# Optimization experiments

Hardware: AMD Instinct MI355X
Metric: run time of the kernel (lower is better)

Reference implementation:

```python
import jax, jax.numpy as jnp
import numpy as np

N_NODES = 50000

def setup_inputs() -> dict:
    key = jax.random.key(0)
    ks = jax.random.split(key, 8)
    input_dim, hidden_dim, output_dim = 128, 256, 64
    x = jax.random.normal(ks[0], (N_NODES, input_dim), dtype=jnp.float32)
    edge_index = jax.random.randint(ks[1], (2, 800000), 0, N_NODES, dtype=jnp.int64)
    s1 = 1.0 / np.sqrt(input_dim)
    s2 = 1.0 / np.sqrt(hidden_dim)
    W1 = jax.random.uniform(ks[2], (input_dim, hidden_dim), jnp.float32, -s1, s1)
    b1 = jax.random.uniform(ks[3], (hidden_dim,), jnp.float32, -s1, s1)
    W2 = jax.random.uniform(ks[4], (hidden_dim, hidden_dim), jnp.float32, -s2, s2)
    b2 = jax.random.uniform(ks[5], (hidden_dim,), jnp.float32, -s2, s2)
    Wc = jax.random.uniform(ks[6], (hidden_dim, output_dim), jnp.float32, -s2, s2)
    bc = jax.random.uniform(ks[7], (output_dim,), jnp.float32, -s2, s2)
    return {"x": x, "edge_index": edge_index, "W1": W1, "b1": b1,
            "W2": W2, "b2": b2, "Wc": Wc, "bc": bc}

def reference(x, edge_index, W1, b1, W2, b2, Wc, bc):
    src, dst = edge_index[0], edge_index[1]
    # GINConv (eps=0): h_i = (1+eps)*x_i + sum_{j->i} x_j
    aggr = jax.ops.segment_sum(x[src], dst, num_segments=N_NODES)  # [N, d_in]
    h = x + aggr
    # 2-layer MLP: Linear -> ReLU -> Linear
    h = jax.nn.relu(h @ W1 + b1) @ W2 + b2  # [N, hidden]
    # classifier on ReLU(conv output)
    return jax.nn.relu(h) @ Wc + bc  # [N, out]
```

## Files before the change

### kernel.cpp

```cpp
#include <hip/hip_runtime.h>
#include <hip/hip_bf16.h>

#define N_NODES 50000
#define M_PAD   50048
#define N_EDGES 800000
#define NBUCK   391
#define NB_EB   391
#define NB_CAST 3125
#define NB_TR   448
#define EBMAX   4096

typedef __bf16 bf16x8 __attribute__((ext_vector_type(8)));
typedef float  f32x4  __attribute__((ext_vector_type(4)));

__device__ __forceinline__ ushort f2bf(float f) {
    __hip_bfloat16 h = __float2bfloat16(f);
    return __builtin_bit_cast(ushort, h);
}
__device__ __forceinline__ float bf2f(ushort u) {
    return __builtin_bit_cast(float, (unsigned)u << 16);
}

__device__ __forceinline__ void gload16(const ushort* g, ushort* l) {
    __builtin_amdgcn_global_load_lds(
        (const __attribute__((address_space(1))) unsigned*)g,
        (__attribute__((address_space(3))) unsigned*)l, 16, 0, 0);
}

__device__ __forceinline__ void transpose_one(const float* W, ushort* WT,
                                              int K, int N, int t) {
    int k = t / N, n = t % N;
    WT[n * K + k] = f2bf(W[t]);
}

__global__ __launch_bounds__(256) void k_prep(const float* __restrict__ x,
                                              ushort* __restrict__ xb,
                                              const float* __restrict__ W1, ushort* __restrict__ W1T,
                                              const float* __restrict__ W2, ushort* __restrict__ W2T,
                                              const float* __restrict__ Wc, ushort* __restrict__ WcT,
                                              int* __restrict__ bcur) {
    int b = blockIdx.x, t = threadIdx.x;
    if (b < NB_CAST) {
        int i = b * 256 + t;
        const float4* x4 = (const float4*)x;
        float4 a = x4[(size_t)i * 2], bb = x4[(size_t)i * 2 + 1];
        ushort o[8];
        o[0] = f2bf(a.x); o[1] = f2bf(a.y); o[2] = f2bf(a.z); o[3] = f2bf(a.w);
        o[4] = f2bf(bb.x); o[5] = f2bf(bb.y); o[6] = f2bf(bb.z); o[7] = f2bf(bb.w);
        *(uint4*)(xb + (size_t)i * 8) = *(uint4*)o;
    } else if (b < NB_CAST + NB_TR) {
        int tg = (b - NB_CAST) * 256 + t;
        const int S1 = 128 * 256, S2 = 256 * 256, S3 = 256 * 64;
        if (tg < S1) transpose_one(W1, W1T, 128, 256, tg);
        else if (tg < S1 + S2) transpose_one(W2, W2T, 256, 256, tg - S1);
        else if (tg < S1 + S2 + S3) transpose_one(Wc, WcT, 256, 64, tg - S1 - S2);
    } else {
        for (int i = t; i < 400; i += 256) bcur[i] = 0;
    }
}

__global__ __launch_bounds__(512) void k_bscatter(const int* __restrict__ ei,
                                                  int* __restrict__ bcur,
                                                  unsigned* __restrict__ pbuf) {
    __shared__ int lh[NBUCK];
    __shared__ int lbase[NBUCK];
    int t = threadIdx.x;
    for (int i = t; i < NBUCK; i += 512) lh[i] = 0;
    __syncthreads();
    int base = blockIdx.x * 2048 + t;
    int s[4], bk[4], rk[4], lo[4];
#pragma unroll
    for (int k = 0; k < 4; ++k) {
        int e = base + k * 512;
        bool ok = e < N_EDGES;
        int ee = ok ? e : 0;
        s[k] = ei[ee];
        int d = ei[N_EDGES + ee];
        bk[k] = ok ? (d >> 7) : -1;
        lo[k] = d & 127;
    }
#pragma unroll
    for (int k = 0; k < 4; ++k)
        if (bk[k] >= 0) rk[k] = atomicAdd(&lh[bk[k]], 1);
    __syncthreads();
    for (int i = t; i < NBUCK; i += 512) {
        int v = lh[i];
        lbase[i] = v ? atomicAdd(&bcur[i], v) : 0;
    }
    __syncthreads();
#pragma unroll
    for (int k = 0; k < 4; ++k)
        if (bk[k] >= 0) {
            int pos = lbase[bk[k]] + rk[k];
            if (pos < EBMAX)
                pbuf[bk[k] * EBMAX + pos] = (unsigned)s[k] | ((unsigned)lo[k] << 17);
        }
}

__global__ __launch_bounds__(256) void k_bplace(const unsigned* __restrict__ pbuf,
                                                const int* __restrict__ bcur,
                                                int* __restrict__ nodestart,
                                                int* __restrict__ nodecnt,
                                                int* __restrict__ elist) {
    __shared__ int lcnt[128], lexc[128], lcur[128];
    int b = blockIdx.x, t = threadIdx.x;
    int m = bcur[b]; if (m > EBMAX) m = EBMAX;
    const unsigned* pb = pbuf + b * EBMAX;
    if (t < 128) lcnt[t] = 0;
    __syncthreads();
    for (int i = t; i < m; i += 256)
        atomicAdd(&lcnt[pb[i] >> 17], 1);
    __syncthreads();
    if (t < 128) lexc[t] = lcnt[t];
    __syncthreads();
#pragma unroll
    for (int off = 1; off < 128; off <<= 1) {
        int u = (t < 128 && t >= off) ? lexc[t - off] : 0;
        __syncthreads();
        if (t < 128) lexc[t] += u;
        __syncthreads();
    }
    if (t < 128) {
        int e = lexc[t] - lcnt[t];
        int node = (b << 7) + t;
        if (node < N_NODES) {
            nodestart[node] = b * EBMAX + e;
            nodecnt[node] = lcnt[t];
        }
        lcur[t] = e;
    }
    __syncthreads();
    for (int i = t; i < m; i += 256) {
        unsigned pr = pb[i];
        int pos = atomicAdd(&lcur[pr >> 17], 1);
        elist[b * EBMAX + pos] = (int)(pr & 0x1FFFF);
    }
}

__global__ __launch_bounds__(256) void k_aggregate(const ushort* __restrict__ xb,
                                                   const int* __restrict__ nodestart,
                                                   const int* __restrict__ nodecnt,
                                                   const int* __restrict__ elist,
                                                   ushort* __restrict__ hsum) {
    int g = threadIdx.x >> 5, lane = threadIdx.x & 31;
    int node = blockIdx.x * 8 + g;
    if (node >= N_NODES) return;
    const ushort4* x4 = (const ushort4*)xb;
    ushort4 mine = x4[(size_t)node * 32 + lane];
    float acc0 = bf2f(mine.x), acc1 = bf2f(mine.y), acc2 = bf2f(mine.z), acc3 = bf2f(mine.w);
    int beg = nodestart[node], cnt = nodecnt[node];
    for (int base = 0; base < cnt; base += 32) {
        int mrem = cnt - base;
        int idx = (lane < mrem) ? elist[beg + base + lane] : 0;
        int c = mrem < 32 ? mrem : 32;
        int j = 0;
        for (; j + 8 <= c; j += 8) {
            ushort4 v[8];
#pragma unroll
            for (int u = 0; u < 8; ++u) {
                int s = __shfl(idx, j + u, 32);
                v[u] = x4[(size_t)s * 32 + lane];
            }
#pragma unroll
            for (int u = 0; u < 8; ++u) {
                acc0 += bf2f(v[u].x); acc1 += bf2f(v[u].y);
                acc2 += bf2f(v[u].z); acc3 += bf2f(v[u].w);
            }
        }
        for (; j < c; ++j) {
            int s = __shfl(idx, j, 32);
            ushort4 v = x4[(size_t)s * 32 + lane];
            acc0 += bf2f(v.x); acc1 += bf2f(v.y); acc2 += bf2f(v.z); acc3 += bf2f(v.w);
        }
    }
    ushort4 o;
    o.x = f2bf(acc0); o.y = f2bf(acc1); o.z = f2bf(acc2); o.w = f2bf(acc3);
    *(ushort4*)(hsum + (size_t)node * 128 + lane * 4) = o;
}

__global__ __launch_bounds__(512) void k_mlp3(const ushort* __restrict__ hsum,
                                              const ushort* __restrict__ W1T,
                                              const float* __restrict__ b1,
                                              const ushort* __restrict__ W2T,
                                              const float* __restrict__ b2,
                                              const ushort* __restrict__ WcT,
                                              const float* __restrict__ bc,
                                              float* __restrict__ out, int M) {
    __shared__ ushort sA[128 * 64];
    __shared__ ushort sB[256 * 64];
    __shared__ ushort ht[128 * 256];

    int m0 = blockIdx.x * 128;
    int tid = threadIdx.x, wv = tid >> 6, lane = tid & 63;
    int lr = lane & 15;
    int kq = (lane >> 4) << 3;
    int l8 = (lane >> 3) & 7, c8 = lane & 7;
    int swz8 = c8 ^ l8;

    int wrow0 = (wv >> 2) * 64;
    int wcol0 = (wv & 3) * 64;
    int crow = (lane >> 4) << 2;

    f32x4 acc[4][4];

#pragma unroll
    for (int m = 0; m < 4; ++m)
#pragma unroll
        for (int n = 0; n < 4; ++n) acc[m][n] = 0;

    for (int kb = 0; kb < 128; kb += 64) {
#pragma unroll
        for (int i = 0; i < 2; ++i) {
            int rg = i * 64 + wv * 8;
            gload16(hsum + (size_t)(m0 + rg + l8) * 128 + kb + swz8 * 8, sA + rg * 64);
        }
#pragma unroll
        for (int i = 0; i < 4; ++i) {
            int rg = i * 64 + wv * 8;
            gload16(W1T + (size_t)(rg + l8) * 128 + kb + swz8 * 8, sB + rg * 64);
        }
        __syncthreads();
#pragma unroll
        for (int kk = 0; kk < 64; kk += 32) {
            int cb = (kk + kq) * 2;
            bf16x8 af[4], bfr[4];
#pragma unroll
            for (int m = 0; m < 4; ++m) {
                int r = wrow0 + m * 16 + lr;
                af[m] = __builtin_bit_cast(bf16x8,
                    *(const uint4*)((const char*)sA + r * 128 + (cb ^ ((r & 7) << 4))));
            }
#pragma unroll
            for (int n = 0; n < 4; ++n) {
                int r = wcol0 + n * 16 + lr;
                bfr[n] = __builtin_bit_cast(bf16x8,
                    *(const uint4*)((const char*)sB + r * 128 + (cb ^ ((r & 7) << 4))));
            }
#pragma unroll
            for (int m = 0; m < 4; ++m)
#pragma unroll
                for (int n = 0; n < 4; ++n)
                    acc[m][n] = __builtin_amdgcn_mfma_f32_16x16x32_bf16(
                        af[m], bfr[n], acc[m][n], 0, 0, 0);
        }
        __syncthreads();
    }
#pragma unroll
    for (int n = 0; n < 4; ++n) {
        int col = wcol0 + n * 16 + lr;
        float bv = b1[col];
#pragma unroll
        for (int m = 0; m < 4; ++m) {
#pragma unroll
            for (int r = 0; r < 4; ++r) {
                int row = wrow0 + m * 16 + crow + r;
                int sc = ((((col >> 3) ^ (row & 7)) << 3) | (col & 7));
                ht[row * 256 + sc] = f2bf(fmaxf(acc[m][n][r] + bv, 0.0f));
            }
        }
    }
    __syncthreads();

#pragma unroll
    for (int m = 0; m < 4; ++m)
#pragma unroll
        for (int n = 0; n < 4; ++n) acc[m][n] = 0;

    for (int kb = 0; kb < 256; kb += 64) {
#pragma unroll
        for (int i = 0; i < 4; ++i) {
            int rg = i * 64 + wv * 8;
            gload16(W2T + (size_t)(rg + l8) * 256 + kb + swz8 * 8, sB + rg * 64);
        }
        __syncthreads();
#pragma unroll
        for (int kk = 0; kk < 64; kk += 32) {
            int cc = kb + kk + kq;
            int cb = (kk + kq) * 2;
            bf16x8 af[4], bfr[4];
#pragma unroll
            for (int m = 0; m < 4; ++m) {
                int r = wrow0 + m * 16 + lr;
                af[m] = __builtin_bit_cast(bf16x8,
                    *(const uint4*)(ht + r * 256 + ((((cc >> 3) ^ (r & 7)) << 3))));
            }
#pragma unroll
            for (int n = 0; n < 4; ++n) {
                int r = wcol0 + n * 16 + lr;
                bfr[n] = __builtin_bit_cast(bf16x8,
                    *(const uint4*)((const char*)sB + r * 128 + (cb ^ ((r & 7) << 4))));
            }
#pragma unroll
            for (int m = 0; m < 4; ++m)
#pragma unroll
                for (int n = 0; n < 4; ++n)
                    acc[m][n] = __builtin_amdgcn_mfma_f32_16x16x32_bf16(
                        af[m], bfr[n], acc[m][n], 0, 0, 0);
        }
        __syncthreads();
    }
#pragma unroll
    for (int n = 0; n < 4; ++n) {
        int col = wcol0 + n * 16 + lr;
        float bv = b2[col];
#pragma unroll
        for (int m = 0; m < 4; ++m) {
#pragma unroll
            for (int r = 0; r < 4; ++r) {
                int row = wrow0 + m * 16 + crow + r;
                int sc = ((((col >> 3) ^ (row & 7)) << 3) | (col & 7));
                ht[row * 256 + sc] = f2bf(fmaxf(acc[m][n][r] + bv, 0.0f));
            }
        }
    }
#pragma unroll
    for (int i = 0; i < 4; ++i)
        gload16(WcT + (size_t)(wv * 8 + l8) * 256 + i * 64 + swz8 * 8,
                sB + i * 4096 + wv * 8 * 64);
    __syncthreads();

    f32x4 acc3[4];
#pragma unroll
    for (int n = 0; n < 4; ++n) acc3[n] = 0;
    int arow3 = wv * 16 + lr;
#pragma unroll
    for (int kb4 = 0; kb4 < 4; ++kb4) {
#pragma unroll
        for (int kk = 0; kk < 64; kk += 32) {
            int cc = kb4 * 64 + kk + kq;
            int cb = (kk + kq) * 2;
            bf16x8 a = __builtin_bit_cast(bf16x8,
                *(const uint4*)(ht + arow3 * 256 + ((((cc >> 3) ^ (arow3 & 7)) << 3))));
#pragma unroll
            for (int n = 0; n < 4; ++n) {
                int r = n * 16 + lr;
                bf16x8 b = __builtin_bit_cast(bf16x8,
                    *(const uint4*)((const char*)sB + kb4 * 8192 + r * 128 +
                                    (cb ^ ((r & 7) << 4))));
                acc3[n] = __builtin_amdgcn_mfma_f32_16x16x32_bf16(a, b, acc3[n], 0, 0, 0);
            }
        }
    }
#pragma unroll
    for (int n = 0; n < 4; ++n) {
        int col = n * 16 + lr;
        float bv = bc[col];
#pragma unroll
        for (int r = 0; r < 4; ++r) {
            int grow = m0 + wv * 16 + crow + r;
            if (grow < M) out[(size_t)grow * 64 + col] = acc3[n][r] + bv;
        }
    }
}


extern "C" void kernel_launch(void* const* d_in, const int* in_sizes, int n_in,
                              void* d_out, int out_size, void* d_ws, size_t ws_size,
                              hipStream_t stream) {
    const float* x  = (const float*)d_in[0];
    const int*   ei = (const int*)d_in[1];
    const float* W1 = (const float*)d_in[2];
    const float* b1 = (const float*)d_in[3];
    const float* W2 = (const float*)d_in[4];
    const float* b2 = (const float*)d_in[5];
    const float* Wc = (const float*)d_in[6];
    const float* bc = (const float*)d_in[7];
    float* out = (float*)d_out;

    char* p = (char*)d_ws;
    int* bcur        = (int*)p; p += 400 * 4;
    int* nodestart   = (int*)p; p += M_PAD * 4;
    int* nodecnt     = (int*)p; p += M_PAD * 4;
    unsigned* pbuf   = (unsigned*)p; p += (size_t)NBUCK * EBMAX * 4;
    int* elist       = (int*)p; p += (size_t)NBUCK * EBMAX * 4;
    ushort* W1T = (ushort*)p; p += 256 * 128 * 2;
    ushort* W2T = (ushort*)p; p += 256 * 256 * 2;
    ushort* WcT = (ushort*)p; p += 64 * 256 * 2;
    ushort* xb  = (ushort*)p; p += (size_t)N_NODES * 128 * 2;
    ushort* hsum = (ushort*)p; p += (size_t)M_PAD * 128 * 2;

    k_prep<<<NB_CAST + NB_TR + 1, 256, 0, stream>>>(x, xb, W1, W1T, W2, W2T, Wc, WcT, bcur);
    k_bscatter<<<NB_EB, 512, 0, stream>>>(ei, bcur, pbuf);
    k_bplace<<<NBUCK, 256, 0, stream>>>(pbuf, bcur, nodestart, nodecnt, elist);
    k_aggregate<<<(N_NODES + 7) / 8, 256, 0, stream>>>(xb, nodestart, nodecnt, elist, hsum);
    k_mlp3<<<M_PAD / 128, 512, 0, stream>>>(hsum, W1T, b1, W2T, b2, WcT, bc, out, N_NODES);
}
```

Before: 101.0 us.

## Halve MLP row tile, widen aggregate unroll, double edges per scatter block

The fused MLP kernel now processes 64 rows per block instead of 128, which doubles the grid and cuts LDS use so that more blocks fit per CU. The warp mapping for the classifier stage is remapped to match. The aggregation loop gathers 16 neighbors per iteration with predicated loads instead of an 8-wide loop plus a scalar tail. The bucket scatter handles 4096 edges per block instead of 2048, giving fewer blocks and fewer global atomics. In exchange, the MLP reloads W1 and W2 from memory twice as often, and the predicated gathers issue wasted slots for nodes with few neighbors.

```diff
diff --git a/kernel.cpp b/kernel.cpp
--- a/kernel.cpp
+++ b/kernel.cpp
@@ -5,7 +5,7 @@
 #define M_PAD   50048
 #define N_EDGES 800000
 #define NBUCK   391
-#define NB_EB   391
+#define NB_EB8  196
 #define NB_CAST 3125
 #define NB_TR   448
 #define EBMAX   4096
@@ -67,10 +67,10 @@
     int t = threadIdx.x;
     for (int i = t; i < NBUCK; i += 512) lh[i] = 0;
     __syncthreads();
-    int base = blockIdx.x * 2048 + t;
-    int s[4], bk[4], rk[4], lo[4];
-#pragma unroll
-    for (int k = 0; k < 4; ++k) {
+    int base = blockIdx.x * 4096 + t;
+    int s[8], bk[8], rk[8], lo[8];
+#pragma unroll
+    for (int k = 0; k < 8; ++k) {
         int e = base + k * 512;
         bool ok = e < N_EDGES;
         int ee = ok ? e : 0;
@@ -80,7 +80,7 @@
         lo[k] = d & 127;
     }
 #pragma unroll
-    for (int k = 0; k < 4; ++k)
+    for (int k = 0; k < 8; ++k)
         if (bk[k] >= 0) rk[k] = atomicAdd(&lh[bk[k]], 1);
     __syncthreads();
     for (int i = t; i < NBUCK; i += 512) {
@@ -89,7 +89,7 @@
     }
     __syncthreads();
 #pragma unroll
-    for (int k = 0; k < 4; ++k)
+    for (int k = 0; k < 8; ++k)
         if (bk[k] >= 0) {
             int pos = lbase[bk[k]] + rk[k];
             if (pos < EBMAX)
@@ -153,24 +153,23 @@
         int mrem = cnt - base;
         int idx = (lane < mrem) ? elist[beg + base + lane] : 0;
         int c = mrem < 32 ? mrem : 32;
-        int j = 0;
-        for (; j + 8 <= c; j += 8) {
-            ushort4 v[8];
-#pragma unroll
-            for (int u = 0; u < 8; ++u) {
-                int s = __shfl(idx, j + u, 32);
-                v[u] = x4[(size_t)s * 32 + lane];
-            }
-#pragma unroll
-            for (int u = 0; u < 8; ++u) {
+        for (int j = 0; j < c; j += 16) {
+            ushort4 v[16];
+#pragma unroll
+            for (int u = 0; u < 16; ++u) {
+                bool ok = (j + u) < c;
+                if (ok) {
+                    int s = __shfl(idx, j + u, 32);
+                    v[u] = x4[(size_t)s * 32 + lane];
+                } else {
+                    v[u] = make_ushort4(0, 0, 0, 0);
+                }
+            }
+#pragma unroll
+            for (int u = 0; u < 16; ++u) {
                 acc0 += bf2f(v[u].x); acc1 += bf2f(v[u].y);
                 acc2 += bf2f(v[u].z); acc3 += bf2f(v[u].w);
             }
-        }
-        for (; j < c; ++j) {
-            int s = __shfl(idx, j, 32);
-            ushort4 v = x4[(size_t)s * 32 + lane];
-            acc0 += bf2f(v.x); acc1 += bf2f(v.y); acc2 += bf2f(v.z); acc3 += bf2f(v.w);
         }
     }
     ushort4 o;
@@ -186,46 +185,42 @@
                                               const ushort* __restrict__ WcT,
                                               const float* __restrict__ bc,
                                               float* __restrict__ out, int M) {
-    __shared__ ushort sA[128 * 64];
+    __shared__ ushort sA[64 * 64];
     __shared__ ushort sB[256 * 64];
-    __shared__ ushort ht[128 * 256];
-
-    int m0 = blockIdx.x * 128;
+    __shared__ ushort ht[64 * 256];
+
+    int m0 = blockIdx.x * 64;
     int tid = threadIdx.x, wv = tid >> 6, lane = tid & 63;
     int lr = lane & 15;
     int kq = (lane >> 4) << 3;
     int l8 = (lane >> 3) & 7, c8 = lane & 7;
     int swz8 = c8 ^ l8;
 
-    int wrow0 = (wv >> 2) * 64;
+    int wrow0 = (wv >> 2) * 32;
     int wcol0 = (wv & 3) * 64;
     int crow = (lane >> 4) << 2;
 
-    f32x4 acc[4][4];
-
-#pragma unroll
-    for (int m = 0; m < 4; ++m)
+    f32x4 acc[2][4];
+
+#pragma unroll
+    for (int m = 0; m < 2; ++m)
 #pragma unroll
         for (int n = 0; n < 4; ++n) acc[m][n] = 0;
 
     for (int kb = 0; kb < 128; kb += 64) {
-#pragma unroll
-        for (int i = 0; i < 2; ++i) {
-            int rg = i * 64 + wv * 8;
-            gload16(hsum + (size_t)(m0 + rg + l8) * 128 + kb + swz8 * 8, sA + rg * 64);
-        }
+        gload16(hsum + (size_t)(m0 + wv * 8 + l8) * 128 + kb + swz8 * 8, sA + wv * 8 * 64);
 #pragma unroll
         for (int i = 0; i < 4; ++i) {
-            int rg = i * 64 + wv * 8;
+            int rg = wv * 32 + i * 8;
             gload16(W1T + (size_t)(rg + l8) * 128 + kb + swz8 * 8, sB + rg * 64);
         }
         __syncthreads();
 #pragma unroll
         for (int kk = 0; kk < 64; kk += 32) {
             int cb = (kk + kq) * 2;
-            bf16x8 af[4], bfr[4];
-#pragma unroll
-            for (int m = 0; m < 4; ++m) {
+            bf16x8 af[2], bfr[4];
+#pragma unroll
+            for (int m = 0; m < 2; ++m) {
                 int r = wrow0 + m * 16 + lr;
                 af[m] = __builtin_bit_cast(bf16x8,
                     *(const uint4*)((const char*)sA + r * 128 + (cb ^ ((r & 7) << 4))));
@@ -237,7 +232,7 @@
                     *(const uint4*)((const char*)sB + r * 128 + (cb ^ ((r & 7) << 4))));
             }
 #pragma unroll
-            for (int m = 0; m < 4; ++m)
+            for (int m = 0; m < 2; ++m)
 #pragma unroll
                 for (int n = 0; n < 4; ++n)
                     acc[m][n] = __builtin_amdgcn_mfma_f32_16x16x32_bf16(
@@ -250,7 +245,7 @@
         int col = wcol0 + n * 16 + lr;
         float bv = b1[col];
 #pragma unroll
-        for (int m = 0; m < 4; ++m) {
+        for (int m = 0; m < 2; ++m) {
 #pragma unroll
             for (int r = 0; r < 4; ++r) {
                 int row = wrow0 + m * 16 + crow + r;
@@ -262,14 +257,14 @@
     __syncthreads();
 
 #pragma unroll
-    for (int m = 0; m < 4; ++m)
+    for (int m = 0; m < 2; ++m)
 #pragma unroll
         for (int n = 0; n < 4; ++n) acc[m][n] = 0;
 
     for (int kb = 0; kb < 256; kb += 64) {
 #pragma unroll
         for (int i = 0; i < 4; ++i) {
-            int rg = i * 64 + wv * 8;
+            int rg = wv * 32 + i * 8;
             gload16(W2T + (size_t)(rg + l8) * 256 + kb + swz8 * 8, sB + rg * 64);
         }
         __syncthreads();
@@ -277,9 +272,9 @@
         for (int kk = 0; kk < 64; kk += 32) {
             int cc = kb + kk + kq;
             int cb = (kk + kq) * 2;
-            bf16x8 af[4], bfr[4];
-#pragma unroll
-            for (int m = 0; m < 4; ++m) {
+            bf16x8 af[2], bfr[4];
+#pragma unroll
+            for (int m = 0; m < 2; ++m) {
                 int r = wrow0 + m * 16 + lr;
                 af[m] = __builtin_bit_cast(bf16x8,
                     *(const uint4*)(ht + r * 256 + ((((cc >> 3) ^ (r & 7)) << 3))));
@@ -291,7 +286,7 @@
                     *(const uint4*)((const char*)sB + r * 128 + (cb ^ ((r & 7) << 4))));
             }
 #pragma unroll
-            for (int m = 0; m < 4; ++m)
+            for (int m = 0; m < 2; ++m)
 #pragma unroll
                 for (int n = 0; n < 4; ++n)
                     acc[m][n] = __builtin_amdgcn_mfma_f32_16x16x32_bf16(
@@ -304,7 +299,7 @@
         int col = wcol0 + n * 16 + lr;
         float bv = b2[col];
 #pragma unroll
-        for (int m = 0; m < 4; ++m) {
+        for (int m = 0; m < 2; ++m) {
 #pragma unroll
             for (int r = 0; r < 4; ++r) {
                 int row = wrow0 + m * 16 + crow + r;
@@ -319,10 +314,12 @@
                 sB + i * 4096 + wv * 8 * 64);
     __syncthreads();
 
-    f32x4 acc3[4];
-#pragma unroll
-    for (int n = 0; n < 4; ++n) acc3[n] = 0;
-    int arow3 = wv * 16 + lr;
+    f32x4 acc3[2];
+#pragma unroll
+    for (int n = 0; n < 2; ++n) acc3[n] = 0;
+    int mrow0 = (wv & 3) * 16;
+    int ncol0 = (wv >> 2) * 32;
+    int arow3 = mrow0 + lr;
 #pragma unroll
     for (int kb4 = 0; kb4 < 4; ++kb4) {
 #pragma unroll
@@ -332,8 +329,8 @@
             bf16x8 a = __builtin_bit_cast(bf16x8,
                 *(const uint4*)(ht + arow3 * 256 + ((((cc >> 3) ^ (arow3 & 7)) << 3))));
 #pragma unroll
-            for (int n = 0; n < 4; ++n) {
-                int r = n * 16 + lr;
+            for (int n = 0; n < 2; ++n) {
+                int r = ncol0 + n * 16 + lr;
                 bf16x8 b = __builtin_bit_cast(bf16x8,
                     *(const uint4*)((const char*)sB + kb4 * 8192 + r * 128 +
                                     (cb ^ ((r & 7) << 4))));
@@ -342,12 +339,12 @@
         }
     }
 #pragma unroll
-    for (int n = 0; n < 4; ++n) {
-        int col = n * 16 + lr;
+    for (int n = 0; n < 2; ++n) {
+        int col = ncol0 + n * 16 + lr;
         float bv = bc[col];
 #pragma unroll
         for (int r = 0; r < 4; ++r) {
-            int grow = m0 + wv * 16 + crow + r;
+            int grow = m0 + mrow0 + crow + r;
             if (grow < M) out[(size_t)grow * 64 + col] = acc3[n][r] + bv;
         }
     }
@@ -380,8 +377,8 @@
     ushort* hsum = (ushort*)p; p += (size_t)M_PAD * 128 * 2;
 
     k_prep<<<NB_CAST + NB_TR + 1, 256, 0, stream>>>(x, xb, W1, W1T, W2, W2T, Wc, WcT, bcur);
-    k_bscatter<<<NB_EB, 512, 0, stream>>>(ei, bcur, pbuf);
+    k_bscatter<<<NB_EB8, 512, 0, stream>>>(ei, bcur, pbuf);
     k_bplace<<<NBUCK, 256, 0, stream>>>(pbuf, bcur, nodestart, nodecnt, elist);
     k_aggregate<<<(N_NODES + 7) / 8, 256, 0, stream>>>(xb, nodestart, nodecnt, elist, hsum);
-    k_mlp3<<<M_PAD / 128, 512, 0, stream>>>(hsum, W1T, b1, W2T, b2, WcT, bc, out, N_NODES);
-}
+    k_mlp3<<<M_PAD / 64, 512, 0, stream>>>(hsum, W1T, b1, W2T, b2, WcT, bc, out, N_NODES);
+}
```

Measured after the change: 102.3 us. Within noise of the previous version (+1.3%).
